# Kernel tuning notes

Hardware: AMD Instinct MI355X
Metric: run time of the kernel (lower is better)

Reference implementation:

```python
import jax, jax.numpy as jnp
import numpy as np

V, BLK, D, H, L = 50257, 2048, 768, 12, 4
HD = D // H
EPS = 1e-5


def _ln(x, w, b):
    mu = jnp.mean(x, axis=-1, keepdims=True)
    var = jnp.mean(jnp.square(x - mu), axis=-1, keepdims=True)
    return (x - mu) * jax.lax.rsqrt(var + EPS) * w + b


def setup_inputs() -> dict:
    key = jax.random.key(0)
    ks = iter(jax.random.split(key, 32))
    s = 0.02
    idx = jax.random.randint(next(ks), (2, 2048), 0, V)
    inp = {
        "idx": idx,
        "wte": jax.random.normal(next(ks), (V, D), jnp.float32) * s,
        "wpe": jax.random.normal(next(ks), (BLK, D), jnp.float32) * s,
        # stacked per-layer params [L, ...]
        "ln1_w": jnp.ones((L, D), jnp.float32),
        "ln1_b": jnp.zeros((L, D), jnp.float32),
        "attn_w": jax.random.normal(next(ks), (L, D, 3 * D), jnp.float32) * s,
        "attn_b": jnp.zeros((L, 3 * D), jnp.float32),
        "proj_w": jax.random.normal(next(ks), (L, D, D), jnp.float32) * (s / np.sqrt(2 * L)),
        "proj_b": jnp.zeros((L, D), jnp.float32),
        "ln2_w": jnp.ones((L, D), jnp.float32),
        "ln2_b": jnp.zeros((L, D), jnp.float32),
        "fc_w": jax.random.normal(next(ks), (L, D, 4 * D), jnp.float32) * s,
        "fc_b": jnp.zeros((L, 4 * D), jnp.float32),
        "fcp_w": jax.random.normal(next(ks), (L, 4 * D, D), jnp.float32) * (s / np.sqrt(2 * L)),
        "fcp_b": jnp.zeros((L, D), jnp.float32),
        "lnf_w": jnp.ones((D,), jnp.float32),
        "lnf_b": jnp.zeros((D,), jnp.float32),
    }
    return inp


def _gpt_forward(idx, wte, wpe, ln1_w, ln1_b, attn_w, attn_b, proj_w, proj_b,
                 ln2_w, ln2_b, fc_w, fc_b, fcp_w, fcp_b, lnf_w, lnf_b):
    B, T = idx.shape
    x = wte[idx] + wpe[:T]  # [B,T,D]; dropout p=0 -> identity
    causal = jnp.tril(jnp.ones((T, T), bool))
    scale = 1.0 / np.sqrt(HD)

    def block(x, p):
        l1w, l1b, aw, ab, pw, pb, l2w, l2b, fw, fb, fpw, fpb = p
        h = _ln(x, l1w, l1b)
        qkv = h @ aw + ab  # [B,T,3D]
        q, k, v = jnp.split(qkv, 3, axis=-1)
        q = q.reshape(B, T, H, HD).transpose(0, 2, 1, 3)  # [B,H,T,hd]
        k = k.reshape(B, T, H, HD).transpose(0, 2, 1, 3)
        v = v.reshape(B, T, H, HD).transpose(0, 2, 1, 3)
        att = jnp.einsum('bhqd,bhkd->bhqk', q, k) * scale
        att = jnp.where(causal, att, -jnp.inf)
        att = jax.nn.softmax(att, axis=-1)
        y = jnp.einsum('bhqk,bhkd->bhqd', att, v)
        y = y.transpose(0, 2, 1, 3).reshape(B, T, D)
        x = x + y @ pw + pb
        h2 = _ln(x, l2w, l2b)
        m = jax.nn.gelu(h2 @ fw + fb, approximate=False) @ fpw + fpb
        return x + m, None

    params = (ln1_w, ln1_b, attn_w, attn_b, proj_w, proj_b,
              ln2_w, ln2_b, fc_w, fc_b, fcp_w, fcp_b)
    x, _ = jax.lax.scan(block, x, params)
    x = _ln(x, lnf_w, lnf_b)
    # inference path: logits only for last position, lm_head tied to wte
    logits = x[:, -1:, :] @ wte.T  # [B,1,V]
    return logits


def reference(idx, wte, wpe, ln1_w, ln1_b, attn_w, attn_b, proj_w, proj_b,
              ln2_w, ln2_b, fc_w, fc_b, fcp_w, fcp_b, lnf_w, lnf_b):
    return _gpt_forward(idx, wte, wpe, ln1_w, ln1_b, attn_w, attn_b, proj_w, proj_b,
                        ln2_w, ln2_b, fc_w, fc_b, fcp_w, fcp_b, lnf_w, lnf_b)
```

## Files before the change

kernel.cpp:

```cpp
#include <hip/hip_runtime.h>
#include <math.h>

#define V 50257
#define B 2
#define T 2048
#define D 768
#define H 12
#define HD 64
#define L 4
#define D3 (3*D)
#define D4 (4*D)
#define NTOK (B*T)
#define EPS 1e-5f

typedef __bf16 v8bf __attribute__((ext_vector_type(8)));
typedef __bf16 v4bf __attribute__((ext_vector_type(4)));
typedef unsigned short v8us __attribute__((ext_vector_type(8)));
typedef float  v4f  __attribute__((ext_vector_type(4)));

#define GAS(p) ((const __attribute__((address_space(1))) void*)(p))
#define LAS(p) ((__attribute__((address_space(3))) void*)(p))

#define LIDX(row, chunk) ((row)*64 + ((((chunk) ^ ((row)&7)))<<3))

#define SBAR() asm volatile("s_barrier" ::: "memory")

__device__ __forceinline__ float gelu_fast(float x) {
    float z  = fabsf(x) * 0.70710678118f;
    float tt = 1.f / (1.f + 0.3275911f * z);
    float poly = tt * (0.254829592f + tt * (-0.284496736f + tt * (1.421413741f +
                 tt * (-1.453152027f + tt * 1.061405429f))));
    float er = 1.f - poly * __expf(-z * z);
    er = (x < 0.f) ? -er : er;
    return 0.5f * x * (1.f + er);
}

__global__ __launch_bounds__(256) void prep_kernel(
        const int* __restrict__ idx, const float* __restrict__ wte,
        const float* __restrict__ wpe, float* __restrict__ x,
        const float* __restrict__ aw_all,  const float* __restrict__ pw_all,
        const float* __restrict__ fw_all,  const float* __restrict__ fpw_all,
        __bf16* __restrict__ awt_all, __bf16* __restrict__ pwt_all,
        __bf16* __restrict__ fwt_all, __bf16* __restrict__ fpwt_all) {
    int bid = blockIdx.x;
    if (bid < 3072) {
        int e = (bid * 256 + threadIdx.x) * 4;
        int pos = e / D;
        int d   = e - pos * D;
        int t   = pos & (T - 1);
        int tok = idx[pos];
        const float4 a  = *(const float4*)(wte + (size_t)tok * D + d);
        const float4 p4 = *(const float4*)(wpe + (size_t)t * D + d);
        float4 r; r.x = a.x + p4.x; r.y = a.y + p4.y; r.z = a.z + p4.z; r.w = a.w + p4.w;
        *(float4*)(x + e) = r;
        return;
    }
    bid -= 3072;
    const int l = bid / 6912; bid -= l * 6912;
    const float* W; __bf16* Wt; int K, N, bx, by;
    if (bid < 1728)      {             W = aw_all  + (size_t)l * D  * D3; Wt = awt_all  + (size_t)l * D3 * D;  K = D;  N = D3; bx = bid % 72; by = bid / 72; }
    else if (bid < 2304) { bid -= 1728; W = pw_all  + (size_t)l * D  * D;  Wt = pwt_all  + (size_t)l * D  * D;  K = D;  N = D;  bx = bid % 24; by = bid / 24; }
    else if (bid < 4608) { bid -= 2304; W = fw_all  + (size_t)l * D  * D4; Wt = fwt_all  + (size_t)l * D4 * D;  K = D;  N = D4; bx = bid % 96; by = bid / 96; }
    else                 { bid -= 4608; W = fpw_all + (size_t)l * D4 * D;  Wt = fpwt_all + (size_t)l * D  * D4; K = D4; N = D;  bx = bid % 24; by = bid / 24; }
    __shared__ float t[32][33];
    const int n0 = bx * 32, k0 = by * 32;
    const int tx = threadIdx.x & 31, ty = threadIdx.x >> 5;
    #pragma unroll
    for (int p = 0; p < 4; ++p)
        t[ty + 8 * p][tx] = W[(size_t)(k0 + ty + 8 * p) * N + n0 + tx];
    __syncthreads();
    #pragma unroll
    for (int p = 0; p < 4; ++p)
        Wt[(size_t)(n0 + ty + 8 * p) * K + k0 + tx] = (__bf16)t[tx][ty + 8 * p];
}

__global__ __launch_bounds__(256) void ln_kernel(const float* __restrict__ X,
                                                 const float* __restrict__ w,
                                                 const float* __restrict__ b,
                                                 __bf16* __restrict__ Y,
                                                 int src_mul, int src_off) {
    int srow = blockIdx.x * src_mul + src_off;
    const float* xr = X + (size_t)srow * D;
    float v[3];
    float s = 0.f, s2 = 0.f;
    #pragma unroll
    for (int j = 0; j < 3; ++j) {
        v[j] = xr[threadIdx.x + 256 * j];
        s += v[j];
        s2 += v[j] * v[j];
    }
    #pragma unroll
    for (int off = 32; off; off >>= 1) {
        s  += __shfl_xor(s, off);
        s2 += __shfl_xor(s2, off);
    }
    __shared__ float ss[4], ss2[4];
    int wave = threadIdx.x >> 6, lane = threadIdx.x & 63;
    if (lane == 0) { ss[wave] = s; ss2[wave] = s2; }
    __syncthreads();
    s  = ss[0] + ss[1] + ss[2] + ss[3];
    s2 = ss2[0] + ss2[1] + ss2[2] + ss2[3];
    float mu  = s * (1.f / D);
    float var = s2 * (1.f / D) - mu * mu;
    float rs  = rsqrtf(var + EPS);
    __bf16* yr = Y + (size_t)blockIdx.x * D;
    #pragma unroll
    for (int j = 0; j < 3; ++j) {
        int c = threadIdx.x + 256 * j;
        yr[c] = (__bf16)((v[j] - mu) * rs * w[c] + b[c]);
    }
}

template<bool DOGELU>
__global__ __launch_bounds__(256) void gemm_bt(const __bf16* __restrict__ A,
                                               const __bf16* __restrict__ Wt,
                                               const float* __restrict__ bias,
                                               __bf16* __restrict__ Cout,
                                               int N, int K) {
    __shared__ __align__(16) __bf16 sm[12288];
    const int tid  = threadIdx.x;
    const int w    = tid >> 6;
    const int lane = tid & 63;

    int fid = blockIdx.y * gridDim.x + blockIdx.x;
    const int nwg = gridDim.x * gridDim.y;
    fid = (fid & 7) * (nwg >> 3) + (fid >> 3);
    const int row0 = (fid / gridDim.x) * 128;
    const int col0 = (fid % gridDim.x) * 64;

    const int srow = ((tid >> 6) & 3) * 16 + (tid & 15);
    const int sk   = ((tid >> 4) & 3) * 8;
    const __bf16* gA0 = A  + (size_t)(row0 + srow) * K + sk;
    const __bf16* gA1 = gA0 + (size_t)64 * K;
    const __bf16* gB0 = Wt + (size_t)(col0 + srow) * K + sk;

    auto stage = [&](int bsel) {
        __bf16* dst = sm + bsel * 6144;
        __builtin_amdgcn_global_load_lds(GAS(gA0), LAS(dst + (size_t)tid * 8), 16, 0, 0);
        __builtin_amdgcn_global_load_lds(GAS(gA1), LAS(dst + (size_t)(tid + 256) * 8), 16, 0, 0);
        __builtin_amdgcn_global_load_lds(GAS(gB0), LAS(dst + 4096 + (size_t)tid * 8), 16, 0, 0);
        gA0 += 32; gA1 += 32; gB0 += 32;
    };

    const int wr = w >> 1, wc = w & 1;
    const __bf16* rA = sm + wr * 2048 + lane * 8;
    const __bf16* rB = sm + 4096 + wc * 1024 + lane * 8;

    const int nt = K >> 5;
    stage(0);

    v4f acc[4][2] = {};
    for (int t = 0; t < nt; ++t) {
        const int cb = (t & 1) * 6144;
        if (t + 1 < nt) {
            stage((t + 1) & 1);
            asm volatile("s_waitcnt vmcnt(3)\n\ts_barrier" ::: "memory");
        } else {
            asm volatile("s_waitcnt vmcnt(0)\n\ts_barrier" ::: "memory");
        }
        v8bf af[4], bfr[2];
        #pragma unroll
        for (int i = 0; i < 4; ++i) af[i]  = *(const v8bf*)(rA + cb + i * 512);
        #pragma unroll
        for (int j = 0; j < 2; ++j) bfr[j] = *(const v8bf*)(rB + cb + j * 512);
        #pragma unroll
        for (int i = 0; i < 4; ++i)
            #pragma unroll
            for (int j = 0; j < 2; ++j)
                acc[i][j] = __builtin_amdgcn_mfma_f32_16x16x32_bf16(af[i], bfr[j], acc[i][j], 0, 0, 0);
        SBAR();
    }

    const int er = (lane >> 4) * 4;
    const int ec = lane & 15;
    #pragma unroll
    for (int j = 0; j < 2; ++j) {
        const int col = wc * 32 + j * 16 + ec;
        const float bval = bias[col0 + col];
        const int chunk = col >> 3, ce = col & 7;
        #pragma unroll
        for (int i = 0; i < 4; ++i) {
            const int rowb = wr * 64 + i * 16 + er;
            #pragma unroll
            for (int rr = 0; rr < 4; ++rr) {
                float vv = acc[i][j][rr] + bval;
                if (DOGELU) vv = gelu_fast(vv);
                sm[LIDX(rowb + rr, chunk) + ce] = (__bf16)vv;
            }
        }
    }
    __syncthreads();
    #pragma unroll
    for (int c = 0; c < 4; ++c) {
        const int chunkid = tid + c * 256;
        const int row = chunkid >> 3;
        const int cc  = chunkid & 7;
        *(v8us*)(void*)(Cout + (size_t)(row0 + row) * N + col0 + cc * 8) =
            *(const v8us*)(const void*)(sm + LIDX(row, cc));
    }
}

__global__ __launch_bounds__(256) void gemm64(const __bf16* __restrict__ A,
                                              const __bf16* __restrict__ Wt,
                                              const float* __restrict__ bias,
                                              const float* __restrict__ res,
                                              float* __restrict__ Cout,
                                              int N, int K) {
    __shared__ __align__(16) __bf16 sm[24576];
    const int tid  = threadIdx.x;
    const int w    = tid >> 6;
    const int lane = tid & 63;

    int fid = blockIdx.y * gridDim.x + blockIdx.x;
    const int nwg = gridDim.x * gridDim.y;
    fid = (fid & 7) * (nwg >> 3) + (fid >> 3);
    const int row0 = (fid / gridDim.x) * 64;
    const int col0 = (fid % gridDim.x) * 64;

    const int srow = ((tid >> 7) & 3) * 16 + (tid & 15);
    const int sk   = ((tid >> 4) & 7) * 8;
    const __bf16* gA0 = A  + (size_t)(row0 + srow) * K + sk;
    const __bf16* gA1 = gA0 + (size_t)32 * K;
    const __bf16* gB0 = Wt + (size_t)(col0 + srow) * K + sk;
    const __bf16* gB1 = gB0 + (size_t)32 * K;

    auto stage = [&](int bsel) {
        __bf16* dst = sm + bsel * 8192;
        __builtin_amdgcn_global_load_lds(GAS(gA0), LAS(dst + (size_t)tid * 8), 16, 0, 0);
        __builtin_amdgcn_global_load_lds(GAS(gA1), LAS(dst + (size_t)(tid + 256) * 8), 16, 0, 0);
        __builtin_amdgcn_global_load_lds(GAS(gB0), LAS(dst + 4096 + (size_t)tid * 8), 16, 0, 0);
        __builtin_amdgcn_global_load_lds(GAS(gB1), LAS(dst + 4096 + (size_t)(tid + 256) * 8), 16, 0, 0);
        gA0 += 64; gA1 += 64; gB0 += 64; gB1 += 64;
    };

    const int wr = w >> 1, wc = w & 1;
    const __bf16* rA = sm + wr * 2048 + lane * 8;
    const __bf16* rB = sm + 4096 + wc * 2048 + lane * 8;

    const int nt = K >> 6;
    stage(0); stage(1);

    v4f acc[2][2] = {};
    for (int t = 0; t < nt; ++t) {
        const int cb = (t % 3) * 8192;
        if (t + 2 < nt) {
            stage((t + 2) % 3);
            asm volatile("s_waitcnt vmcnt(8)\n\ts_barrier" ::: "memory");
        } else if (t + 1 < nt) {
            asm volatile("s_waitcnt vmcnt(4)\n\ts_barrier" ::: "memory");
        } else {
            asm volatile("s_waitcnt vmcnt(0)\n\ts_barrier" ::: "memory");
        }
        #pragma unroll
        for (int h = 0; h < 2; ++h) {
            v8bf af[2], bfr[2];
            #pragma unroll
            for (int i = 0; i < 2; ++i) af[i]  = *(const v8bf*)(rA + cb + i * 1024 + h * 512);
            #pragma unroll
            for (int j = 0; j < 2; ++j) bfr[j] = *(const v8bf*)(rB + cb + j * 1024 + h * 512);
            #pragma unroll
            for (int i = 0; i < 2; ++i)
                #pragma unroll
                for (int j = 0; j < 2; ++j)
                    acc[i][j] = __builtin_amdgcn_mfma_f32_16x16x32_bf16(af[i], bfr[j], acc[i][j], 0, 0, 0);
        }
        SBAR();
    }

    float* smf = (float*)sm;
    const int er = (lane >> 4) * 4;
    const int ec = lane & 15;
    #pragma unroll
    for (int j = 0; j < 2; ++j) {
        const int col = wc * 32 + j * 16 + ec;
        const float bval = bias[col0 + col];
        #pragma unroll
        for (int i = 0; i < 2; ++i) {
            #pragma unroll
            for (int rr = 0; rr < 4; ++rr) {
                const int row = wr * 32 + i * 16 + er + rr;
                smf[row * 64 + (col ^ ((row & 3) << 4))] = acc[i][j][rr] + bval;
            }
        }
    }
    __syncthreads();
    #pragma unroll
    for (int c = 0; c < 4; ++c) {
        const int chunkid = tid + c * 256;
        const int row = chunkid >> 4;
        const int c0  = (chunkid & 15) * 4;
        float4 vv = *(const float4*)(smf + row * 64 + (c0 ^ ((row & 3) << 4)));
        const float4 rv = *(const float4*)(res + (size_t)(row0 + row) * N + col0 + c0);
        vv.x += rv.x; vv.y += rv.y; vv.z += rv.z; vv.w += rv.w;
        *(float4*)(Cout + (size_t)(row0 + row) * N + col0 + c0) = vv;
    }
}

__global__ __launch_bounds__(256) void attn_mfma(const __bf16* __restrict__ qkv,
                                                 __bf16* __restrict__ y) {
    __shared__ __align__(16) __bf16 Qs[4096];
    __shared__ __align__(16) __bf16 Ks[4096];
    __shared__ __align__(16) __bf16 Vt[4096];
    __shared__ __align__(16) __bf16 Ps[4][1024];

    const int tid  = threadIdx.x;
    const int w    = tid >> 6;
    const int lane = tid & 63;
    const int quad = lane >> 4;
    const int l4   = lane & 15;

    int fid = blockIdx.x;
    const int nwg = gridDim.x;
    fid = (fid & 7) * (nwg >> 3) + (fid >> 3);

    const int qt = 31 - (fid & 31);
    const int bh = fid >> 5;
    const int b  = bh / H;
    const int h  = bh - b * H;
    const int q0 = qt * 64;

    const __bf16* base = qkv + (size_t)(b * T) * D3 + h * HD;

    {
        int c = tid;
        #pragma unroll
        for (int rep = 0; rep < 2; ++rep, c += 256) {
            int row = c >> 3, ch = c & 7;
            v8us v = *(const v8us*)(const void*)(base + (size_t)(q0 + row) * D3 + ch * 8);
            *(v8us*)(void*)(Qs + LIDX(row, ch)) = v;
        }
    }

    const int krow = tid >> 3, kch = tid & 7;
    const int vkp = tid & 31, vdc = tid >> 5;
    const __bf16* kp0 = base + D     + (size_t)krow * D3 + kch * 8;
    const __bf16* kp1 = kp0 + (size_t)32 * D3;
    const __bf16* vp0 = base + 2 * D + (size_t)(2 * vkp) * D3 + vdc * 8;
    const __bf16* vp1 = vp0 + D3;

    v8us kr0 = *(const v8us*)(const void*)kp0;
    v8us kr1 = *(const v8us*)(const void*)kp1;
    v8us vr0 = *(const v8us*)(const void*)vp0;
    v8us vr1 = *(const v8us*)(const void*)vp1;

    float m_local = -INFINITY;
    v4f o[4] = {};
    v4f sacc = {};
    v8bf qf[2];
    v8bf vones;
    #pragma unroll
    for (int i = 0; i < 8; ++i) vones[i] = (__bf16)1.0f;

    const int nt = qt + 1;
    const size_t adv = (size_t)64 * D3;
    const int qrow = q0 + w * 16 + l4;

    for (int kt = 0; kt < nt; ++kt) {
        const int k0 = kt * 64;
        *(v8us*)(void*)(Ks + LIDX(krow, kch))      = kr0;
        *(v8us*)(void*)(Ks + LIDX(krow + 32, kch)) = kr1;
        #pragma unroll
        for (int j = 0; j < 8; ++j) {
            int dim = vdc * 8 + j;
            int idx = dim * 64 + ((((vkp >> 2) ^ (dim & 7))) << 3) + ((vkp & 3) << 1);
            *(unsigned int*)(void*)(Vt + idx) =
                ((unsigned int)vr1[j] << 16) | (unsigned int)vr0[j];
        }
        __syncthreads();

        if (kt == 0) {
            #pragma unroll
            for (int kh = 0; kh < 2; ++kh)
                qf[kh] = *(const v8bf*)(Qs + LIDX(w * 16 + l4, kh * 4 + quad));
        }
        if (kt + 1 < nt) {
            kp0 += adv; kp1 += adv; vp0 += adv; vp1 += adv;
            kr0 = *(const v8us*)(const void*)kp0;
            kr1 = *(const v8us*)(const void*)kp1;
            vr0 = *(const v8us*)(const void*)vp0;
            vr1 = *(const v8us*)(const void*)vp1;
        }

        v4f s[4] = {};
        __builtin_amdgcn_s_setprio(1);
        #pragma unroll
        for (int kh = 0; kh < 2; ++kh) {
            #pragma unroll
            for (int jb = 0; jb < 4; ++jb) {
                v8bf bk = *(const v8bf*)(Ks + LIDX(jb * 16 + l4, kh * 4 + quad));
                s[jb] = __builtin_amdgcn_mfma_f32_16x16x32_bf16(bk, qf[kh], s[jb], 0, 0, 0);
            }
        }
        __builtin_amdgcn_s_setprio(0);

        float sv[4][4];
        float mx = -INFINITY;
        #pragma unroll
        for (int jb = 0; jb < 4; ++jb) {
            #pragma unroll
            for (int rg = 0; rg < 4; ++rg) {
                float vvv = s[jb][rg] * 0.125f;
                if (k0 + jb * 16 + quad * 4 + rg > qrow) vvv = -INFINITY;
                sv[jb][rg] = vvv;
                mx = fmaxf(mx, vvv);
            }
        }
        mx = fmaxf(mx, __shfl_xor(mx, 16));
        mx = fmaxf(mx, __shfl_xor(mx, 32));
        if (!__all(mx <= m_local + 8.f)) {
            const float mnew    = fmaxf(m_local, mx);
            const float alpha_l = __expf(m_local - mnew);
            m_local = mnew;
            float a4[4];
            #pragma unroll
            for (int r = 0; r < 4; ++r) a4[r] = __shfl(alpha_l, quad * 4 + r);
            #pragma unroll
            for (int r = 0; r < 4; ++r) {
                sacc[r] *= a4[r];
                #pragma unroll
                for (int db = 0; db < 4; ++db) o[db][r] *= a4[r];
            }
        }
        #pragma unroll
        for (int jb = 0; jb < 4; ++jb) {
            v4bf pk;
            #pragma unroll
            for (int rg = 0; rg < 4; ++rg)
                pk[rg] = (__bf16)__expf(sv[jb][rg] - m_local);
            *(v4bf*)(void*)(&Ps[w][LIDX(l4, jb * 2 + (quad >> 1)) + ((quad & 1) << 2)]) = pk;
        }
        __builtin_amdgcn_s_setprio(1);
        #pragma unroll
        for (int kh = 0; kh < 2; ++kh) {
            v8bf ap = *(const v8bf*)(&Ps[w][LIDX(l4, kh * 4 + quad)]);
            sacc = __builtin_amdgcn_mfma_f32_16x16x32_bf16(ap, vones, sacc, 0, 0, 0);
            #pragma unroll
            for (int db = 0; db < 4; ++db) {
                v8bf bv = *(const v8bf*)(Vt + LIDX(db * 16 + l4, kh * 4 + quad));
                o[db] = __builtin_amdgcn_mfma_f32_16x16x32_bf16(ap, bv, o[db], 0, 0, 0);
            }
        }
        __builtin_amdgcn_s_setprio(0);
        __syncthreads();
    }

    #pragma unroll
    for (int db = 0; db < 4; ++db) {
        #pragma unroll
        for (int r = 0; r < 4; ++r) {
            const int q = q0 + w * 16 + quad * 4 + r;
            y[(size_t)(b * T + q) * D + h * HD + db * 16 + l4] =
                (__bf16)(o[db][r] / sacc[r]);
        }
    }
}

__global__ __launch_bounds__(256) void logits_kernel(const __bf16* __restrict__ xf,
                                                     const float* __restrict__ wte,
                                                     float* __restrict__ out) {
    int wave = threadIdx.x >> 6;
    int lane = threadIdx.x & 63;
    int v = blockIdx.x * 4 + wave;
    if (v >= V) return;
    const float4* wr = (const float4*)(wte + (size_t)v * D);
    const v4bf*   x0 = (const v4bf*)(xf);
    const v4bf*   x1 = (const v4bf*)(xf + D);
    float s0 = 0.f, s1 = 0.f;
    #pragma unroll
    for (int j = 0; j < 3; ++j) {
        float4 wv = wr[lane + 64 * j];
        v4bf a0 = x0[lane + 64 * j];
        v4bf a1 = x1[lane + 64 * j];
        s0 = fmaf(wv.x, (float)a0[0], s0); s0 = fmaf(wv.y, (float)a0[1], s0);
        s0 = fmaf(wv.z, (float)a0[2], s0); s0 = fmaf(wv.w, (float)a0[3], s0);
        s1 = fmaf(wv.x, (float)a1[0], s1); s1 = fmaf(wv.y, (float)a1[1], s1);
        s1 = fmaf(wv.z, (float)a1[2], s1); s1 = fmaf(wv.w, (float)a1[3], s1);
    }
    #pragma unroll
    for (int off = 32; off; off >>= 1) {
        s0 += __shfl_xor(s0, off);
        s1 += __shfl_xor(s1, off);
    }
    if (lane == 0) { out[v] = s0; out[V + v] = s1; }
}

extern "C" void kernel_launch(void* const* d_in, const int* in_sizes, int n_in,
                              void* d_out, int out_size, void* d_ws, size_t ws_size,
                              hipStream_t stream) {
    const int*   idx    = (const int*)  d_in[0];
    const float* wte    = (const float*)d_in[1];
    const float* wpe    = (const float*)d_in[2];
    const float* ln1_w  = (const float*)d_in[3];
    const float* ln1_b  = (const float*)d_in[4];
    const float* attn_w = (const float*)d_in[5];
    const float* attn_b = (const float*)d_in[6];
    const float* proj_w = (const float*)d_in[7];
    const float* proj_b = (const float*)d_in[8];
    const float* ln2_w  = (const float*)d_in[9];
    const float* ln2_b  = (const float*)d_in[10];
    const float* fc_w   = (const float*)d_in[11];
    const float* fc_b   = (const float*)d_in[12];
    const float* fcp_w  = (const float*)d_in[13];
    const float* fcp_b  = (const float*)d_in[14];
    const float* lnf_w  = (const float*)d_in[15];
    const float* lnf_b  = (const float*)d_in[16];
    float* out = (float*)d_out;

    char* ws = (char*)d_ws;
    float*  x    = (float*)ws;  ws += (size_t)NTOK * D  * 4;
    __bf16* qkvb = (__bf16*)ws;
    __bf16* gb   = (__bf16*)ws; ws += (size_t)NTOK * D4 * 2;
    __bf16* hb   = (__bf16*)ws; ws += (size_t)NTOK * D  * 2;
    __bf16* yb   = (__bf16*)ws; ws += (size_t)NTOK * D  * 2;
    __bf16* awt  = (__bf16*)ws; ws += (size_t)L * D3 * D   * 2;
    __bf16* pwt  = (__bf16*)ws; ws += (size_t)L * D  * D   * 2;
    __bf16* fwt  = (__bf16*)ws; ws += (size_t)L * D4 * D   * 2;
    __bf16* fpwt = (__bf16*)ws; ws += (size_t)L * D  * D4  * 2;
    __bf16* xf   = (__bf16*)ws; ws += (size_t)B * D    * 2;

    prep_kernel<<<3072 + 6912 * L, 256, 0, stream>>>(idx, wte, wpe, x,
                                                     attn_w, proj_w, fc_w, fcp_w,
                                                     awt, pwt, fwt, fpwt);

    for (int l = 0; l < L; ++l) {
        const float* l1w = ln1_w + l * D;
        const float* l1b = ln1_b + l * D;
        const float* ab  = attn_b + l * D3;
        const float* pb  = proj_b + l * D;
        const float* l2w = ln2_w + l * D;
        const float* l2b = ln2_b + l * D;
        const float* fb  = fc_b + l * D4;
        const float* fpb = fcp_b + l * D;
        const __bf16* awl  = awt  + (size_t)l * D3 * D;
        const __bf16* pwl  = pwt  + (size_t)l * D  * D;
        const __bf16* fwl  = fwt  + (size_t)l * D4 * D;
        const __bf16* fpwl = fpwt + (size_t)l * D  * D4;

        ln_kernel<<<NTOK, 256, 0, stream>>>(x, l1w, l1b, hb, 1, 0);
        gemm_bt<false><<<dim3(D3 / 64, NTOK / 128), 256, 0, stream>>>(
            hb, awl, ab, qkvb, D3, D);
        attn_mfma<<<B * H * (T / 64), 256, 0, stream>>>(qkvb, yb);
        gemm64<<<dim3(D / 64, NTOK / 64), 256, 0, stream>>>(
            yb, pwl, pb, x, x, D, D);
        ln_kernel<<<NTOK, 256, 0, stream>>>(x, l2w, l2b, hb, 1, 0);
        gemm_bt<true><<<dim3(D4 / 64, NTOK / 128), 256, 0, stream>>>(
            hb, fwl, fb, gb, D4, D);
        gemm64<<<dim3(D / 64, NTOK / 64), 256, 0, stream>>>(
            gb, fpwl, fpb, x, x, D, D4);
    }

    ln_kernel<<<B, 256, 0, stream>>>(x, lnf_w, lnf_b, xf, T, T - 1);
    logits_kernel<<<(V + 3) / 4, 256, 0, stream>>>(xf, wte, out);
}
```

Baseline: 1.332 ms.

## Replace 128x64 bf16 GEMM with 256x256-tile 512-thread kernel for QKV and FC

Replaces the QKV and FC projection GEMM with a larger-tile kernel: 256x256 output tiles per 512-thread workgroup, each wave computing a 128x64 sub-tile with 8x4 MFMA accumulators. The larger tile gives more reuse of each LDS-loaded operand per MFMA and cuts global traffic. The epilogue is staged through LDS in two halves with a new swizzle. In exchange the grid becomes small (9x16 or 12x16 workgroups, fewer than the CU count), and register pressure is higher, which can lower occupancy and latency hiding.

```diff
diff --git a/kernel.cpp b/kernel.cpp
--- a/kernel.cpp
+++ b/kernel.cpp
@@ -22,6 +22,7 @@
 #define LAS(p) ((__attribute__((address_space(3))) void*)(p))
 
 #define LIDX(row, chunk) ((row)*64 + ((((chunk) ^ ((row)&7)))<<3))
+#define C2IDX(row, chunk) ((row)*256 + ((((chunk) ^ (((row)&7)<<2)))<<3))
 
 #define SBAR() asm volatile("s_barrier" ::: "memory")
 
@@ -112,91 +113,109 @@
 }
 
 template<bool DOGELU>
-__global__ __launch_bounds__(256) void gemm_bt(const __bf16* __restrict__ A,
+__global__ __launch_bounds__(512) void gemm256(const __bf16* __restrict__ A,
                                                const __bf16* __restrict__ Wt,
                                                const float* __restrict__ bias,
                                                __bf16* __restrict__ Cout,
                                                int N, int K) {
-    __shared__ __align__(16) __bf16 sm[12288];
+    __shared__ __align__(16) __bf16 sm[32768];
     const int tid  = threadIdx.x;
     const int w    = tid >> 6;
     const int lane = tid & 63;
+    const int wm   = w >> 2;
+    const int wn   = w & 3;
 
     int fid = blockIdx.y * gridDim.x + blockIdx.x;
     const int nwg = gridDim.x * gridDim.y;
     fid = (fid & 7) * (nwg >> 3) + (fid >> 3);
-    const int row0 = (fid / gridDim.x) * 128;
-    const int col0 = (fid % gridDim.x) * 64;
-
-    const int srow = ((tid >> 6) & 3) * 16 + (tid & 15);
-    const int sk   = ((tid >> 4) & 3) * 8;
-    const __bf16* gA0 = A  + (size_t)(row0 + srow) * K + sk;
-    const __bf16* gA1 = gA0 + (size_t)64 * K;
-    const __bf16* gB0 = Wt + (size_t)(col0 + srow) * K + sk;
+    const int row0 = (fid / gridDim.x) * 256;
+    const int col0 = (fid % gridDim.x) * 256;
+
+    const int l15 = lane & 15;
+    const int lq8 = (lane >> 4) * 8;
+    const __bf16* gAsrc[2];
+    const __bf16* gBsrc[2];
+    {
+        #pragma unroll
+        for (int rep = 0; rep < 2; ++rep) {
+            int ga = w * 2 + rep;
+            int awm = ga >> 3, ai = ga & 7;
+            gAsrc[rep] = A + (size_t)(row0 + awm * 128 + ai * 16 + l15) * K + lq8;
+            int gb = w * 2 + rep;
+            int bwn = gb >> 2, bj = gb & 3;
+            gBsrc[rep] = Wt + (size_t)(col0 + bwn * 64 + bj * 16 + l15) * K + lq8;
+        }
+    }
 
     auto stage = [&](int bsel) {
-        __bf16* dst = sm + bsel * 6144;
-        __builtin_amdgcn_global_load_lds(GAS(gA0), LAS(dst + (size_t)tid * 8), 16, 0, 0);
-        __builtin_amdgcn_global_load_lds(GAS(gA1), LAS(dst + (size_t)(tid + 256) * 8), 16, 0, 0);
-        __builtin_amdgcn_global_load_lds(GAS(gB0), LAS(dst + 4096 + (size_t)tid * 8), 16, 0, 0);
-        gA0 += 32; gA1 += 32; gB0 += 32;
+        __bf16* dst = sm + bsel * 16384;
+        #pragma unroll
+        for (int rep = 0; rep < 2; ++rep) {
+            const int g = w * 2 + rep;
+            __builtin_amdgcn_global_load_lds(GAS(gAsrc[rep]), LAS(dst + (size_t)(g * 64 + lane) * 8), 16, 0, 0);
+            __builtin_amdgcn_global_load_lds(GAS(gBsrc[rep]), LAS(dst + 8192 + (size_t)(g * 64 + lane) * 8), 16, 0, 0);
+            gAsrc[rep] += 32; gBsrc[rep] += 32;
+        }
     };
-
-    const int wr = w >> 1, wc = w & 1;
-    const __bf16* rA = sm + wr * 2048 + lane * 8;
-    const __bf16* rB = sm + 4096 + wc * 1024 + lane * 8;
 
     const int nt = K >> 5;
     stage(0);
 
-    v4f acc[4][2] = {};
+    v4f acc[8][4] = {};
     for (int t = 0; t < nt; ++t) {
-        const int cb = (t & 1) * 6144;
+        const int cb = (t & 1) * 16384;
         if (t + 1 < nt) {
             stage((t + 1) & 1);
-            asm volatile("s_waitcnt vmcnt(3)\n\ts_barrier" ::: "memory");
+            asm volatile("s_waitcnt vmcnt(4)\n\ts_barrier" ::: "memory");
         } else {
             asm volatile("s_waitcnt vmcnt(0)\n\ts_barrier" ::: "memory");
         }
-        v8bf af[4], bfr[2];
-        #pragma unroll
-        for (int i = 0; i < 4; ++i) af[i]  = *(const v8bf*)(rA + cb + i * 512);
-        #pragma unroll
-        for (int j = 0; j < 2; ++j) bfr[j] = *(const v8bf*)(rB + cb + j * 512);
-        #pragma unroll
-        for (int i = 0; i < 4; ++i)
-            #pragma unroll
-            for (int j = 0; j < 2; ++j)
-                acc[i][j] = __builtin_amdgcn_mfma_f32_16x16x32_bf16(af[i], bfr[j], acc[i][j], 0, 0, 0);
+        v8bf bf[4];
+        #pragma unroll
+        for (int j = 0; j < 4; ++j)
+            bf[j] = *(const v8bf*)(sm + cb + 8192 + (size_t)((wn * 4 + j) * 64 + lane) * 8);
+        #pragma unroll
+        for (int i = 0; i < 8; ++i) {
+            v8bf af = *(const v8bf*)(sm + cb + (size_t)((wm * 8 + i) * 64 + lane) * 8);
+            #pragma unroll
+            for (int j = 0; j < 4; ++j)
+                acc[i][j] = __builtin_amdgcn_mfma_f32_16x16x32_bf16(af, bf[j], acc[i][j], 0, 0, 0);
+        }
         SBAR();
     }
 
     const int er = (lane >> 4) * 4;
     const int ec = lane & 15;
     #pragma unroll
-    for (int j = 0; j < 2; ++j) {
-        const int col = wc * 32 + j * 16 + ec;
-        const float bval = bias[col0 + col];
-        const int chunk = col >> 3, ce = col & 7;
-        #pragma unroll
-        for (int i = 0; i < 4; ++i) {
-            const int rowb = wr * 64 + i * 16 + er;
-            #pragma unroll
-            for (int rr = 0; rr < 4; ++rr) {
-                float vv = acc[i][j][rr] + bval;
-                if (DOGELU) vv = gelu_fast(vv);
-                sm[LIDX(rowb + rr, chunk) + ce] = (__bf16)vv;
+    for (int half = 0; half < 2; ++half) {
+        if (wm == half) {
+            #pragma unroll
+            for (int j = 0; j < 4; ++j) {
+                const int col = wn * 64 + j * 16 + ec;
+                const float bval = bias[col0 + col];
+                const int chunk = col >> 3, ce = col & 7;
+                #pragma unroll
+                for (int i = 0; i < 8; ++i) {
+                    const int rowb = i * 16 + er;
+                    #pragma unroll
+                    for (int rr = 0; rr < 4; ++rr) {
+                        float vv = acc[i][j][rr] + bval;
+                        if (DOGELU) vv = gelu_fast(vv);
+                        sm[C2IDX(rowb + rr, chunk) + ce] = (__bf16)vv;
+                    }
+                }
             }
         }
-    }
-    __syncthreads();
-    #pragma unroll
-    for (int c = 0; c < 4; ++c) {
-        const int chunkid = tid + c * 256;
-        const int row = chunkid >> 3;
-        const int cc  = chunkid & 7;
-        *(v8us*)(void*)(Cout + (size_t)(row0 + row) * N + col0 + cc * 8) =
-            *(const v8us*)(const void*)(sm + LIDX(row, cc));
+        __syncthreads();
+        #pragma unroll
+        for (int c = 0; c < 8; ++c) {
+            const int chunkid = tid + c * 512;
+            const int row = chunkid >> 5;
+            const int cc  = chunkid & 31;
+            *(v8us*)(void*)(Cout + (size_t)(row0 + half * 128 + row) * N + col0 + cc * 8) =
+                *(const v8us*)(const void*)(sm + C2IDX(row, cc));
+        }
+        __syncthreads();
     }
 }
 
@@ -537,13 +556,13 @@
         const __bf16* fpwl = fpwt + (size_t)l * D  * D4;
 
         ln_kernel<<<NTOK, 256, 0, stream>>>(x, l1w, l1b, hb, 1, 0);
-        gemm_bt<false><<<dim3(D3 / 64, NTOK / 128), 256, 0, stream>>>(
+        gemm256<false><<<dim3(D3 / 256, NTOK / 256), 512, 0, stream>>>(
             hb, awl, ab, qkvb, D3, D);
         attn_mfma<<<B * H * (T / 64), 256, 0, stream>>>(qkvb, yb);
         gemm64<<<dim3(D / 64, NTOK / 64), 256, 0, stream>>>(
             yb, pwl, pb, x, x, D, D);
         ln_kernel<<<NTOK, 256, 0, stream>>>(x, l2w, l2b, hb, 1, 0);
-        gemm_bt<true><<<dim3(D4 / 64, NTOK / 128), 256, 0, stream>>>(
+        gemm256<true><<<dim3(D4 / 256, NTOK / 256), 512, 0, stream>>>(
             hb, fwl, fb, gb, D4, D);
         gemm64<<<dim3(D / 64, NTOK / 64), 256, 0, stream>>>(
             gb, fpwl, fpb, x, x, D, D4);
```

Result: faster. 1.280 ms (-3.9%).
